# Kernel optimization log

Hardware: AMD Instinct MI355X
Metric: run time of the kernel (lower is better)

## Reference

```python
import jax, jax.numpy as jnp
import numpy as np

CD_WEIGHT = 1.0
EMD_WEIGHT = 1.0
EPS = 1e-3        # sinkhorn entropic regularization (matches eps=0.001)
ITERS = 50        # matches max_iters=50 (stop_thresh ignored: fixed trip count for jit)
NEG = -1e9        # log(0) stand-in for padded points
BIG = 1e10        # +inf stand-in for masked chamfer distances


def _sqdist(x, y):
    # x [N,3], y [M,3] -> squared euclidean distances [N,M]  (p=2 cost)
    return jnp.maximum(
        jnp.sum(x * x, -1)[:, None] + jnp.sum(y * y, -1)[None, :] - 2.0 * (x @ y.T),
        0.0,
    )


def _sinkhorn_cost(x, y, n, m):
    # Log-domain Sinkhorn OT cost between one padded pair: x [N,3], y [M,3],
    # with n, m valid points and uniform marginals 1/n, 1/m on valid points.
    N, M = x.shape[0], y.shape[0]
    C = _sqdist(x, y)
    nf = n.astype(jnp.float32)
    mf = m.astype(jnp.float32)
    log_a = jnp.where(jnp.arange(N) < n, -jnp.log(nf), NEG)  # [N]
    log_b = jnp.where(jnp.arange(M) < m, -jnp.log(mf), NEG)  # [M]

    def body(_, fg):
        f, g = fg
        f = -EPS * jax.scipy.special.logsumexp(log_b[None, :] + (g[None, :] - C) / EPS, axis=1)
        g = -EPS * jax.scipy.special.logsumexp(log_a[:, None] + (f[:, None] - C) / EPS, axis=0)
        return (f, g)

    f, g = jax.lax.fori_loop(0, ITERS, body, (jnp.zeros(N), jnp.zeros(M)))
    log_P = log_a[:, None] + log_b[None, :] + (f[:, None] + g[None, :] - C) / EPS
    return jnp.sum(jnp.exp(log_P) * C)


def _chamfer(px, gy, n_len, m_len):
    # pytorch3d chamfer_distance with point_reduction='mean', batch_reduction='mean'
    # px [B,N,3], gy [B,M,3]; n_len/m_len [B] float valid counts.
    B, N, _ = px.shape
    M = gy.shape[1]
    D = jnp.maximum(
        jnp.sum(px * px, -1)[:, :, None]
        + jnp.sum(gy * gy, -1)[:, None, :]
        - 2.0 * jnp.einsum('bnd,bmd->bnm', px, gy),
        0.0,
    )  # [B,N,M]
    mx = jnp.arange(N)[None, :] < n_len[:, None]  # [B,N]
    my = jnp.arange(M)[None, :] < m_len[:, None]  # [B,M]
    dx = jnp.min(jnp.where(my[:, None, :], D, BIG), axis=2)  # [B,N] NN dist x->y
    dy = jnp.min(jnp.where(mx[:, :, None], D, BIG), axis=1)  # [B,M] NN dist y->x
    cham_x = jnp.sum(jnp.where(mx, dx, 0.0), axis=1) / n_len.astype(jnp.float32)
    cham_y = jnp.sum(jnp.where(my, dy, 0.0), axis=1) / m_len.astype(jnp.float32)
    return jnp.mean(cham_x + cham_y)


def setup_inputs() -> dict:
    key = jax.random.key(0)
    k1, k2, k3, k4 = jax.random.split(key, 4)
    B, N, M = 8, 2048, 2048
    pred_points = 0.5 * jax.random.normal(k1, (B, N, 3), dtype=jnp.float32)
    gt_points = 0.5 * jax.random.normal(k2, (B, M, 3), dtype=jnp.float32)
    pred_lengths = jax.random.randint(k3, (B,), N // 2, N + 1, dtype=jnp.int32)
    gt_lengths = jax.random.randint(k4, (B,), M // 2, M + 1, dtype=jnp.int32)
    return {
        'pred_points': pred_points,
        'gt_points': gt_points,
        'pred_lengths': pred_lengths,
        'gt_lengths': gt_lengths,
    }


def reference(pred_points, gt_points, pred_lengths, gt_lengths):
    # Original clips extracted points to [-1, 1] before losses.
    px = jnp.clip(pred_points, -1.0, 1.0)
    gy = jnp.clip(gt_points, -1.0, 1.0)
    # EMD: per-sample sinkhorn cost, sqrt, mean over samples, weighted.
    emd_costs = jax.vmap(_sinkhorn_cost)(px, gy, pred_lengths, gt_lengths)  # [B]
    emd_loss = EMD_WEIGHT * jnp.mean(jnp.sqrt(emd_costs))
    # Chamfer on padded clouds with lengths.
    cd_loss = CD_WEIGHT * _chamfer(px, gy, pred_lengths.astype(jnp.float32), gt_lengths.astype(jnp.float32))
    return cd_loss + emd_loss
```

## Files before the change

kernel.cpp:

```cpp
#include <hip/hip_runtime.h>

#define BATCH 8
#define NPTS  2048
#define TPB   512
#define WGB   64
#define NWG   (BATCH*WGB)
#define ITERS 50
#define R     4

#define KLOG2E    1442.6950408889634f
#define TWO_K     2885.3900817779268f
#define INV_TK    3.4657359027997264e-4f
#define INV_K     6.931471805599453e-4f
#define INV_2K_SQ 1.2011325347955035e-7f
#define AR_SCALE  -1.7328679513998632e-4f
#define NEGU      -1e30f
#define BIGD      1e10f

typedef float f2 __attribute__((ext_vector_type(2)));

__device__ __forceinline__ float exp2fast(float x) { return __builtin_amdgcn_exp2f(x); }
__device__ __forceinline__ float log2fast(float x) { return __builtin_amdgcn_logf(x); }
__device__ __forceinline__ float clipf(float v)    { return fminf(fmaxf(v, -1.0f), 1.0f); }
__device__ __forceinline__ f2 bc(float x) { f2 r; r.x = x; r.y = x; return r; }

__device__ __forceinline__ f2 pk_fma(f2 a, f2 b, f2 c) {
    f2 d;
    asm("v_pk_fma_f32 %0, %1, %2, %3" : "=v"(d) : "v"(a), "v"(b), "v"(c));
    return d;
}
__device__ __forceinline__ f2 pk_add(f2 a, f2 b) {
    f2 d;
    asm("v_pk_add_f32 %0, %1, %2" : "=v"(d) : "v"(a), "v"(b));
    return d;
}

__device__ __forceinline__ float aloadf(const float* p) {
    return __hip_atomic_load(p, __ATOMIC_RELAXED, __HIP_MEMORY_SCOPE_AGENT);
}
__device__ __forceinline__ void astoref(float* p, float v) {
    __hip_atomic_store(p, v, __ATOMIC_RELAXED, __HIP_MEMORY_SCOPE_AGENT);
}
__device__ __forceinline__ int aloadi(const int* p) {
    return __hip_atomic_load(p, __ATOMIC_RELAXED, __HIP_MEMORY_SCOPE_AGENT);
}
__device__ __forceinline__ void astorei(int* p, int v) {
    __hip_atomic_store(p, v, __ATOMIC_RELAXED, __HIP_MEMORY_SCOPE_AGENT);
}

__device__ __forceinline__ float wsum(float v) {
#pragma unroll
    for (int d = 1; d < 64; d <<= 1) v += __shfl_xor(v, d);
    return v;
}
__device__ __forceinline__ float wmax(float v) {
#pragma unroll
    for (int d = 1; d < 64; d <<= 1) v = fmaxf(v, __shfl_xor(v, d));
    return v;
}
__device__ __forceinline__ float wmin(float v) {
#pragma unroll
    for (int d = 1; d < 64; d <<= 1) v = fminf(v, __shfl_xor(v, d));
    return v;
}

__device__ __forceinline__ void batch_barrier(int* subs_base, int* sub, int* top,
                                              int* gen, int tid)
{
    __syncthreads();
    if (tid == 0) {
        asm volatile("s_waitcnt vmcnt(0)" ::: "memory");
        int g = aloadi(gen);
        int a = __hip_atomic_fetch_add(sub, 1, __ATOMIC_RELAXED, __HIP_MEMORY_SCOPE_AGENT);
        if (a == 7) {
            int t = __hip_atomic_fetch_add(top, 1, __ATOMIC_RELAXED, __HIP_MEMORY_SCOPE_AGENT);
            if (t == 7) {
#pragma unroll
                for (int s = 0; s < 8; ++s) astorei(subs_base + s * 16, 0);
                astorei(top, 0);
                asm volatile("s_waitcnt vmcnt(0)" ::: "memory");
                astorei(gen, g + 1);
            } else {
                while (aloadi(gen) == g) __builtin_amdgcn_s_sleep(1);
            }
        } else {
            while (aloadi(gen) == g) __builtin_amdgcn_s_sleep(1);
        }
    }
    __syncthreads();
}

__device__ __forceinline__ void half_fused_pk(
    const f2* __restrict__ cx, const f2* __restrict__ cy,
    const f2* __restrict__ cz, const f2* __restrict__ cw,
    const f2* __restrict__ rx, const f2* __restrict__ ry, const f2* __restrict__ rz,
    float* __restrict__ uout, float L2C, float* L, float* D,
    int nrows, int ncols, int r0, int lane)
{
    if (r0 >= nrows) return;
    const int nst = (ncols + 127) >> 7;
    const int rp = r0 >> 1;
    f2 vx0 = rx[rp], vx1 = rx[rp + 1];
    f2 vy0 = ry[rp], vy1 = ry[rp + 1];
    f2 vz0 = rz[rp], vz1 = rz[rp + 1];
    f2 x0p[R] = { bc(vx0.x * INV_TK), bc(vx0.y * INV_TK), bc(vx1.x * INV_TK), bc(vx1.y * INV_TK) };
    f2 x1p[R] = { bc(vy0.x * INV_TK), bc(vy0.y * INV_TK), bc(vy1.x * INV_TK), bc(vy1.y * INV_TK) };
    f2 x2p[R] = { bc(vz0.x * INV_TK), bc(vz0.y * INV_TK), bc(vz1.x * INV_TK), bc(vz1.y * INV_TK) };

    float Lp[R];
    f2 nLp[R];
#pragma unroll
    for (int r = 0; r < R; ++r) { Lp[r] = L[r] + D[r]; nLp[r] = bc(-Lp[r]); }

    float S0[R], S1[R];
#pragma unroll
    for (int r = 0; r < R; ++r) { S0[r] = 0.0f; S1[r] = 0.0f; }

    for (int s = 0; s < nst; ++s) {
        int p = (s << 6) + lane;
        f2 bx = cx[p], by = cy[p], bz = cz[p], bw = cw[p];
#pragma unroll
        for (int r = 0; r < R; ++r) {
            f2 t = pk_fma(x2p[r], bz, bw);
            t = pk_fma(x1p[r], by, t);
            t = pk_fma(x0p[r], bx, t);
            t = pk_add(nLp[r], t);
            S0[r] += exp2fast(t.x);
            S1[r] += exp2fast(t.y);
        }
    }

    float Ssum[R];
    bool redo = false;
#pragma unroll
    for (int r = 0; r < R; ++r) {
        Ssum[r] = wsum(S0[r] + S1[r]);
        redo |= !(Ssum[r] >= 1e-30f && Ssum[r] <= 1e30f);
    }
    if (redo) {
        float Mn[R];
#pragma unroll
        for (int r = 0; r < R; ++r) Mn[r] = -3.0e38f;
        for (int s = 0; s < nst; ++s) {
            int p = (s << 6) + lane;
            f2 bx = cx[p], by = cy[p], bz = cz[p], bw = cw[p];
#pragma unroll
            for (int r = 0; r < R; ++r) {
                f2 t = pk_fma(x2p[r], bz, bw);
                t = pk_fma(x1p[r], by, t);
                t = pk_fma(x0p[r], bx, t);
                Mn[r] = fmaxf(Mn[r], fmaxf(t.x, t.y));
            }
        }
#pragma unroll
        for (int r = 0; r < R; ++r) {
            Lp[r] = wmax(Mn[r]); nLp[r] = bc(-Lp[r]);
            S0[r] = 0.0f; S1[r] = 0.0f;
        }
        for (int s = 0; s < nst; ++s) {
            int p = (s << 6) + lane;
            f2 bx = cx[p], by = cy[p], bz = cz[p], bw = cw[p];
#pragma unroll
            for (int r = 0; r < R; ++r) {
                f2 t = pk_fma(x2p[r], bz, bw);
                t = pk_fma(x1p[r], by, t);
                t = pk_fma(x0p[r], bx, t);
                t = pk_add(nLp[r], t);
                S0[r] += exp2fast(t.x);
                S1[r] += exp2fast(t.y);
            }
        }
#pragma unroll
        for (int r = 0; r < R; ++r) Ssum[r] = wsum(S0[r] + S1[r]);
    }

    float uv[R];
#pragma unroll
    for (int r = 0; r < R; ++r) {
        float lnew = Lp[r] + log2fast(Ssum[r]);
        D[r] = (L[r] > 1.0e37f) ? 0.0f : (lnew - L[r]);
        L[r] = lnew;
        uv[r] = L2C - lnew;
    }
    float v = uv[0];
#pragma unroll
    for (int r = 1; r < R; ++r) v = (lane == r) ? uv[r] : v;
    if (lane < R && (r0 + lane) < nrows) astoref(&uout[r0 + lane], v);
}

__launch_bounds__(TPB, 4)
__global__ void pcl_kernel(const float* __restrict__ pred,
                           const float* __restrict__ gt,
                           const int* __restrict__ nlen,
                           const int* __restrict__ mlen,
                           int* __restrict__ hdr,
                           float* __restrict__ fbuf,
                           float* __restrict__ gbuf,
                           float* __restrict__ parts,
                           float* __restrict__ bres,
                           float* __restrict__ out)
{
    __shared__ f2 XSX[NPTS/2], XSY[NPTS/2], XSZ[NPTS/2], XSW[NPTS/2];
    __shared__ f2 YSX[NPTS/2], YSY[NPTS/2], YSZ[NPTS/2], YSW[NPTS/2];

    const int tid  = threadIdx.x;
    const int wg   = blockIdx.x;
    const int lo   = wg & 255;
    const int hi   = wg >> 8;
    const int b    = ((lo & 7) + hi) & 7;
    const int wloc = (lo >> 3) + hi * 32;
    const int wv   = tid >> 6;
    const int lane = tid & 63;
    const int r0   = wloc * 32 + wv * R;
    const int n = nlen[b];
    const int m = mlen[b];
    const float nf = (float)n, mf = (float)m;
    const float* predb = pred + (size_t)b * NPTS * 3;
    const float* gtb   = gt   + (size_t)b * NPTS * 3;
    float* fb = fbuf + b * NPTS;
    float* gb = gbuf + b * NPTS;
    int* subs_base = hdr + b * 128;
    int* sub       = subs_base + (wloc >> 3) * 16;
    int* top       = hdr + (64 + b) * 16;
    int* gen       = hdr + (72 + b) * 16;
    int* done      = hdr + 80 * 16;

    for (int idx = tid; idx < NPTS; idx += TPB) {
        const float* p = predb + (size_t)idx * 3;
        ((float*)XSX)[idx] = clipf(p[0]) * TWO_K;
        ((float*)XSY)[idx] = clipf(p[1]) * TWO_K;
        ((float*)XSZ)[idx] = clipf(p[2]) * TWO_K;
        const float* q = gtb + (size_t)idx * 3;
        ((float*)YSX)[idx] = clipf(q[0]) * TWO_K;
        ((float*)YSY)[idx] = clipf(q[1]) * TWO_K;
        ((float*)YSZ)[idx] = clipf(q[2]) * TWO_K;
    }
    __syncthreads();

    const float L2M = log2fast(mf);
    const float L2N = log2fast(nf);

    float Lf[R], Lg[R], Df[R], Dg[R];
#pragma unroll
    for (int r = 0; r < R; ++r) {
        Lf[r] = 3.0e38f; Lg[r] = 3.0e38f;
        Df[r] = 0.0f;    Dg[r] = 0.0f;
    }

    for (int it = 0; it < ITERS; ++it) {
        if (it == 0) {
            for (int j = tid; j < NPTS; j += TPB) {
                float sx = ((float*)YSX)[j], sy = ((float*)YSY)[j], sz = ((float*)YSZ)[j];
                float u0 = AR_SCALE * fmaf(sx, sx, fmaf(sy, sy, sz * sz));
                ((float*)YSW)[j] = (j < m) ? u0 : NEGU;
            }
        } else {
            for (int j = tid; j < NPTS; j += TPB)
                ((float*)YSW)[j] = (j < m) ? aloadf(&gb[j]) : NEGU;
        }
        __syncthreads();
        half_fused_pk(YSX, YSY, YSZ, YSW, XSX, XSY, XSZ, fb, L2M, Lf, Df, n, m, r0, lane);
        batch_barrier(subs_base, sub, top, gen, tid);
        for (int i = tid; i < NPTS; i += TPB)
            ((float*)XSW)[i] = (i < n) ? aloadf(&fb[i]) : NEGU;
        __syncthreads();
        half_fused_pk(XSX, XSY, XSZ, XSW, YSX, YSY, YSZ, gb, L2N, Lg, Dg, m, n, r0, lane);
        batch_barrier(subs_base, sub, top, gen, tid);
    }

    for (int j = tid; j < NPTS; j += TPB)
        ((float*)YSW)[j] = (j < m) ? aloadf(&gb[j]) : NEGU;
    __syncthreads();

    float wcost = 0.0f, chx = 0.0f;
    if (r0 < n) {
        const int rp = r0 >> 1;
        f2 vx0 = XSX[rp], vx1 = XSX[rp + 1];
        f2 vy0 = XSY[rp], vy1 = XSY[rp + 1];
        f2 vz0 = XSZ[rp], vz1 = XSZ[rp + 1];
        float px0[R] = { vx0.x * INV_TK, vx0.y * INV_TK, vx1.x * INV_TK, vx1.y * INV_TK };
        float px1[R] = { vy0.x * INV_TK, vy0.y * INV_TK, vy1.x * INV_TK, vy1.y * INV_TK };
        float px2[R] = { vz0.x * INV_TK, vz0.y * INV_TK, vz1.x * INV_TK, vz1.y * INV_TK };
        float pxx[R], hrow[R];
        f2 dmn[R];
#pragma unroll
        for (int r = 0; r < R; ++r) {
            float sx = px0[r] * TWO_K, sy = px1[r] * TWO_K, sz = px2[r] * TWO_K;
            pxx[r] = fmaf(sx, sx, fmaf(sy, sy, sz * sz)) * INV_2K_SQ;
            hrow[r] = (r0 + r < n) ? aloadf(&fb[r0 + r]) : NEGU;
            dmn[r].x = BIGD; dmn[r].y = BIGD;
        }
        const int nst = (m + 127) >> 7;
        for (int s = 0; s < nst; ++s) {
            int p = (s << 6) + lane;
            f2 bx = YSX[p], by = YSY[p], bz = YSZ[p], bw = YSW[p];
            f2 yy2 = (bx * bx + by * by + bz * bz) * INV_2K_SQ;
            bool jv0 = (2 * p)     < m;
            bool jv1 = (2 * p + 1) < m;
#pragma unroll
            for (int r = 0; r < R; ++r) {
                f2 dots = px0[r] * bx + px1[r] * by + px2[r] * bz;
                f2 e = dots + bw + hrow[r];
                float w0 = exp2fast(e.x), w1 = exp2fast(e.y);
                f2 C;
                C.x = fmaxf(fmaf(dots.x, -INV_K, pxx[r] + yy2.x), 0.0f);
                C.y = fmaxf(fmaf(dots.y, -INV_K, pxx[r] + yy2.y), 0.0f);
                wcost = fmaf(w0, C.x, fmaf(w1, C.y, wcost));
                dmn[r].x = fminf(dmn[r].x, jv0 ? C.x : BIGD);
                dmn[r].y = fminf(dmn[r].y, jv1 ? C.y : BIGD);
            }
        }
#pragma unroll
        for (int r = 0; r < R; ++r) {
            float d = wmin(fminf(dmn[r].x, dmn[r].y));
            if (r0 + r < n) chx += d;
        }
        wcost = wsum(wcost);
    }

    float chy = 0.0f;
    if (r0 < m) {
        const int rp = r0 >> 1;
        f2 vx0 = YSX[rp], vx1 = YSX[rp + 1];
        f2 vy0 = YSY[rp], vy1 = YSY[rp + 1];
        f2 vz0 = YSZ[rp], vz1 = YSZ[rp + 1];
        float qy0[R] = { vx0.x * INV_TK, vx0.y * INV_TK, vx1.x * INV_TK, vx1.y * INV_TK };
        float qy1[R] = { vy0.x * INV_TK, vy0.y * INV_TK, vy1.x * INV_TK, vy1.y * INV_TK };
        float qy2[R] = { vz0.x * INV_TK, vz0.y * INV_TK, vz1.x * INV_TK, vz1.y * INV_TK };
        float qyy[R];
        f2 dmn[R];
#pragma unroll
        for (int r = 0; r < R; ++r) {
            float sx = qy0[r] * TWO_K, sy = qy1[r] * TWO_K, sz = qy2[r] * TWO_K;
            qyy[r] = fmaf(sx, sx, fmaf(sy, sy, sz * sz)) * INV_2K_SQ;
            dmn[r].x = BIGD; dmn[r].y = BIGD;
        }
        const int nst = (n + 127) >> 7;
        for (int s = 0; s < nst; ++s) {
            int p = (s << 6) + lane;
            f2 bx = XSX[p], by = XSY[p], bz = XSZ[p];
            f2 xx2 = (bx * bx + by * by + bz * bz) * INV_2K_SQ;
            bool iv0 = (2 * p)     < n;
            bool iv1 = (2 * p + 1) < n;
#pragma unroll
            for (int r = 0; r < R; ++r) {
                f2 dots = qy0[r] * bx + qy1[r] * by + qy2[r] * bz;
                f2 C;
                C.x = fmaxf(fmaf(dots.x, -INV_K, qyy[r] + xx2.x), 0.0f);
                C.y = fmaxf(fmaf(dots.y, -INV_K, qyy[r] + xx2.y), 0.0f);
                dmn[r].x = fminf(dmn[r].x, iv0 ? C.x : BIGD);
                dmn[r].y = fminf(dmn[r].y, iv1 ? C.y : BIGD);
            }
        }
#pragma unroll
        for (int r = 0; r < R; ++r) {
            float d = wmin(fminf(dmn[r].x, dmn[r].y));
            if (r0 + r < m) chy += d;
        }
    }
    __syncthreads();

    float* xs = (float*)XSX;
    if (lane == 0) { xs[wv] = wcost; xs[8 + wv] = chx; xs[16 + wv] = chy; }
    __syncthreads();
    if (tid == 0) {
        float cs = 0.0f, cx = 0.0f, cy = 0.0f;
        for (int w = 0; w < 8; ++w) { cs += xs[w]; cx += xs[8 + w]; cy += xs[16 + w]; }
        astoref(&parts[(b * WGB + wloc) * 4 + 0], cs);
        astoref(&parts[(b * WGB + wloc) * 4 + 1], cx);
        astoref(&parts[(b * WGB + wloc) * 4 + 2], cy);
    }
    batch_barrier(subs_base, sub, top, gen, tid);

    if (wloc == 0 && wv == 0) {
        float cs = aloadf(&parts[(b * WGB + lane) * 4 + 0]);
        float cx = aloadf(&parts[(b * WGB + lane) * 4 + 1]);
        float cy = aloadf(&parts[(b * WGB + lane) * 4 + 2]);
        cs = wsum(cs); cx = wsum(cx); cy = wsum(cy);
        if (lane == 0) {
            float cost = cs / (nf * mf);
            astoref(&bres[b], sqrtf(fmaxf(cost, 0.0f)) + cx / nf + cy / mf);
            asm volatile("s_waitcnt vmcnt(0)" ::: "memory");
            int a = __hip_atomic_fetch_add(done, 1, __ATOMIC_RELAXED, __HIP_MEMORY_SCOPE_AGENT);
            if (a == BATCH - 1) {
                float acc = 0.0f;
                for (int i2 = 0; i2 < BATCH; ++i2) acc += aloadf(&bres[i2]);
                out[0] = acc * 0.125f;
            }
        }
    }
}

extern "C" void kernel_launch(void* const* d_in, const int* in_sizes, int n_in,
                              void* d_out, int out_size, void* d_ws, size_t ws_size,
                              hipStream_t stream) {
    const float* pred = (const float*)d_in[0];
    const float* gt   = (const float*)d_in[1];
    const int*  nlen  = (const int*)d_in[2];
    const int*  mlen  = (const int*)d_in[3];

    int*   hdr   = (int*)d_ws;
    float* base  = (float*)d_ws + 2048;
    float* fbuf  = base;
    float* gbuf  = fbuf + BATCH * NPTS;
    float* parts = gbuf + BATCH * NPTS;
    float* bres  = parts + NWG * 4;
    float* out   = (float*)d_out;

    hipMemsetAsync(d_ws, 0, 8192, stream);
    hipLaunchKernelGGL(pcl_kernel, dim3(NWG), dim3(TPB), 0, stream,
                       pred, gt, nlen, mlen, hdr, fbuf, gbuf, parts, bres, out);
}
```

Measured before the change: 806.2 us.

## Replace per-batch global barriers with per-producer dataflow flags

Swaps the hierarchical batch-wide barrier for per-workgroup progress flags. Each thread now waits only on the single producer workgroup whose f/g slice it loads, using 64-bit loads into a float4 LDS buffer. The workgroup-to-batch mapping is also simplified to b = wg & 7. The aim is to remove full barrier latency and let workgroups run ahead. The risk is that correctness now depends on memory ordering with relaxed atomics, since flag stores are not preceded by explicit vmcnt waits. Flags are also never reset between launches, so repeated calls would see stale counts unless the host clears hdr.

```diff
diff --git a/kernel.cpp b/kernel.cpp
--- a/kernel.cpp
+++ b/kernel.cpp
@@ -47,6 +47,11 @@
 __device__ __forceinline__ void astorei(int* p, int v) {
     __hip_atomic_store(p, v, __ATOMIC_RELAXED, __HIP_MEMORY_SCOPE_AGENT);
 }
+__device__ __forceinline__ f2 aloadf2(const float* p) {
+    unsigned long long v = __hip_atomic_load((const unsigned long long*)p,
+                                             __ATOMIC_RELAXED, __HIP_MEMORY_SCOPE_AGENT);
+    union { unsigned long long u; f2 f; } c; c.u = v; return c.f;
+}
 
 __device__ __forceinline__ float wsum(float v) {
 #pragma unroll
@@ -64,30 +69,8 @@
     return v;
 }
 
-__device__ __forceinline__ void batch_barrier(int* subs_base, int* sub, int* top,
-                                              int* gen, int tid)
-{
-    __syncthreads();
-    if (tid == 0) {
-        asm volatile("s_waitcnt vmcnt(0)" ::: "memory");
-        int g = aloadi(gen);
-        int a = __hip_atomic_fetch_add(sub, 1, __ATOMIC_RELAXED, __HIP_MEMORY_SCOPE_AGENT);
-        if (a == 7) {
-            int t = __hip_atomic_fetch_add(top, 1, __ATOMIC_RELAXED, __HIP_MEMORY_SCOPE_AGENT);
-            if (t == 7) {
-#pragma unroll
-                for (int s = 0; s < 8; ++s) astorei(subs_base + s * 16, 0);
-                astorei(top, 0);
-                asm volatile("s_waitcnt vmcnt(0)" ::: "memory");
-                astorei(gen, g + 1);
-            } else {
-                while (aloadi(gen) == g) __builtin_amdgcn_s_sleep(1);
-            }
-        } else {
-            while (aloadi(gen) == g) __builtin_amdgcn_s_sleep(1);
-        }
-    }
-    __syncthreads();
+__device__ __forceinline__ void waitflag(const int* p, int target) {
+    while (aloadi(p) < target) __builtin_amdgcn_s_sleep(1);
 }
 
 __device__ __forceinline__ void half_fused_pk(
@@ -200,15 +183,14 @@
                            float* __restrict__ bres,
                            float* __restrict__ out)
 {
-    __shared__ f2 XSX[NPTS/2], XSY[NPTS/2], XSZ[NPTS/2], XSW[NPTS/2];
-    __shared__ f2 YSX[NPTS/2], YSY[NPTS/2], YSZ[NPTS/2], YSW[NPTS/2];
+    __shared__ f2 XSX[NPTS/2], XSY[NPTS/2], XSZ[NPTS/2];
+    __shared__ f2 YSX[NPTS/2], YSY[NPTS/2], YSZ[NPTS/2];
+    __shared__ float4 XW[TPB], YW[TPB];
 
     const int tid  = threadIdx.x;
     const int wg   = blockIdx.x;
-    const int lo   = wg & 255;
-    const int hi   = wg >> 8;
-    const int b    = ((lo & 7) + hi) & 7;
-    const int wloc = (lo >> 3) + hi * 32;
+    const int b    = wg & 7;
+    const int wloc = wg >> 3;
     const int wv   = tid >> 6;
     const int lane = tid & 63;
     const int r0   = wloc * 32 + wv * R;
@@ -219,11 +201,10 @@
     const float* gtb   = gt   + (size_t)b * NPTS * 3;
     float* fb = fbuf + b * NPTS;
     float* gb = gbuf + b * NPTS;
-    int* subs_base = hdr + b * 128;
-    int* sub       = subs_base + (wloc >> 3) * 16;
-    int* top       = hdr + (64 + b) * 16;
-    int* gen       = hdr + (72 + b) * 16;
-    int* done      = hdr + 80 * 16;
+    int* flagF = hdr + b * WGB;
+    int* flagG = hdr + 512 + b * WGB;
+    int* cntb  = hdr + 1024 + b * 16;
+    int* done  = hdr + 1152;
 
     for (int idx = tid; idx < NPTS; idx += TPB) {
         const float* p = predb + (size_t)idx * 3;
@@ -239,6 +220,8 @@
 
     const float L2M = log2fast(mf);
     const float L2N = log2fast(nf);
+    const int j0 = tid << 2;
+    const int myprod = tid >> 3;
 
     float Lf[R], Lg[R], Df[R], Dg[R];
 #pragma unroll
@@ -248,32 +231,75 @@
     }
 
     for (int it = 0; it < ITERS; ++it) {
-        if (it == 0) {
-            for (int j = tid; j < NPTS; j += TPB) {
-                float sx = ((float*)YSX)[j], sy = ((float*)YSY)[j], sz = ((float*)YSZ)[j];
-                float u0 = AR_SCALE * fmaf(sx, sx, fmaf(sy, sy, sz * sz));
-                ((float*)YSW)[j] = (j < m) ? u0 : NEGU;
-            }
-        } else {
-            for (int j = tid; j < NPTS; j += TPB)
-                ((float*)YSW)[j] = (j < m) ? aloadf(&gb[j]) : NEGU;
+        {
+            float4 w;
+            if (it == 0) {
+                f2 gx0 = YSX[2*tid], gy0 = YSY[2*tid], gz0 = YSZ[2*tid];
+                f2 gx1 = YSX[2*tid+1], gy1 = YSY[2*tid+1], gz1 = YSZ[2*tid+1];
+                f2 s0 = gx0*gx0 + gy0*gy0 + gz0*gz0;
+                f2 s1 = gx1*gx1 + gy1*gy1 + gz1*gz1;
+                w.x = s0.x * AR_SCALE; w.y = s0.y * AR_SCALE;
+                w.z = s1.x * AR_SCALE; w.w = s1.y * AR_SCALE;
+            } else {
+                waitflag(&flagG[myprod], it);
+                f2 a = aloadf2(&gb[j0]);
+                f2 c = aloadf2(&gb[j0 + 2]);
+                w.x = a.x; w.y = a.y; w.z = c.x; w.w = c.y;
+            }
+            if (j0 + 3 >= m) {
+                if (j0     >= m) w.x = NEGU;
+                if (j0 + 1 >= m) w.y = NEGU;
+                if (j0 + 2 >= m) w.z = NEGU;
+                w.w = NEGU;
+            }
+            YW[tid] = w;
         }
         __syncthreads();
-        half_fused_pk(YSX, YSY, YSZ, YSW, XSX, XSY, XSZ, fb, L2M, Lf, Df, n, m, r0, lane);
-        batch_barrier(subs_base, sub, top, gen, tid);
-        for (int i = tid; i < NPTS; i += TPB)
-            ((float*)XSW)[i] = (i < n) ? aloadf(&fb[i]) : NEGU;
+        half_fused_pk(YSX, YSY, YSZ, (const f2*)YW, XSX, XSY, XSZ,
+                      fb, L2M, Lf, Df, n, m, r0, lane);
         __syncthreads();
-        half_fused_pk(XSX, XSY, XSZ, XSW, YSX, YSY, YSZ, gb, L2N, Lg, Dg, m, n, r0, lane);
-        batch_barrier(subs_base, sub, top, gen, tid);
-    }
-
-    for (int j = tid; j < NPTS; j += TPB)
-        ((float*)YSW)[j] = (j < m) ? aloadf(&gb[j]) : NEGU;
+        if (tid == 0) astorei(&flagF[wloc], it + 1);
+
+        {
+            waitflag(&flagF[myprod], it + 1);
+            f2 a = aloadf2(&fb[j0]);
+            f2 c = aloadf2(&fb[j0 + 2]);
+            float4 w;
+            w.x = a.x; w.y = a.y; w.z = c.x; w.w = c.y;
+            if (j0 + 3 >= n) {
+                if (j0     >= n) w.x = NEGU;
+                if (j0 + 1 >= n) w.y = NEGU;
+                if (j0 + 2 >= n) w.z = NEGU;
+                w.w = NEGU;
+            }
+            XW[tid] = w;
+        }
+        __syncthreads();
+        half_fused_pk(XSX, XSY, XSZ, (const f2*)XW, YSX, YSY, YSZ,
+                      gb, L2N, Lg, Dg, m, n, r0, lane);
+        __syncthreads();
+        if (tid == 0) astorei(&flagG[wloc], it + 1);
+    }
+
+    {
+        waitflag(&flagG[myprod], ITERS);
+        f2 a = aloadf2(&gb[j0]);
+        f2 c = aloadf2(&gb[j0 + 2]);
+        float4 w;
+        w.x = a.x; w.y = a.y; w.z = c.x; w.w = c.y;
+        if (j0 + 3 >= m) {
+            if (j0     >= m) w.x = NEGU;
+            if (j0 + 1 >= m) w.y = NEGU;
+            if (j0 + 2 >= m) w.z = NEGU;
+            w.w = NEGU;
+        }
+        YW[tid] = w;
+    }
     __syncthreads();
 
     float wcost = 0.0f, chx = 0.0f;
     if (r0 < n) {
+        const f2* YWf = (const f2*)YW;
         const int rp = r0 >> 1;
         f2 vx0 = XSX[rp], vx1 = XSX[rp + 1];
         f2 vy0 = XSY[rp], vy1 = XSY[rp + 1];
@@ -293,7 +319,7 @@
         const int nst = (m + 127) >> 7;
         for (int s = 0; s < nst; ++s) {
             int p = (s << 6) + lane;
-            f2 bx = YSX[p], by = YSY[p], bz = YSZ[p], bw = YSW[p];
+            f2 bx = YSX[p], by = YSY[p], bz = YSZ[p], bw = YWf[p];
             f2 yy2 = (bx * bx + by * by + bz * bz) * INV_2K_SQ;
             bool jv0 = (2 * p)     < m;
             bool jv1 = (2 * p + 1) < m;
@@ -369,10 +395,12 @@
         astoref(&parts[(b * WGB + wloc) * 4 + 0], cs);
         astoref(&parts[(b * WGB + wloc) * 4 + 1], cx);
         astoref(&parts[(b * WGB + wloc) * 4 + 2], cy);
-    }
-    batch_barrier(subs_base, sub, top, gen, tid);
+        asm volatile("s_waitcnt vmcnt(0)" ::: "memory");
+        __hip_atomic_fetch_add(cntb, 1, __ATOMIC_RELAXED, __HIP_MEMORY_SCOPE_AGENT);
+    }
 
     if (wloc == 0 && wv == 0) {
+        while (aloadi(cntb) < WGB) __builtin_amdgcn_s_sleep(1);
         float cs = aloadf(&parts[(b * WGB + lane) * 4 + 0]);
         float cx = aloadf(&parts[(b * WGB + lane) * 4 + 1]);
         float cy = aloadf(&parts[(b * WGB + lane) * 4 + 2]);
```

Measured after the change: 1.204 ms. 49.3% more time.
